# Kernel optimization log

Hardware: AMD Instinct MI355X
Metric: run time of the kernel (lower is better)

Reference implementation:

```python
import jax, jax.numpy as jnp
import numpy as np

K = 7          # kernel_size
DIL = 1        # dilation
TOPK = 8       # top_k
EPS = 1e-8     # torch cosine_similarity eps
W_SRC_POS = W_SRC_NEG = W_SIM_POS = W_SIM_NEG = 1.0


def unfold(x):
    # x: [B, C, H, W] -> [B, C, K*K, H, W]  (torch nn.Unfold ordering: c, kh, kw)
    B, C, H, W = x.shape
    pad = (K // 2) * DIL
    xp = jnp.pad(x, ((0, 0), (0, 0), (pad, pad), (pad, pad)))
    pats = [xp[:, :, i * DIL:i * DIL + H, j * DIL:j * DIL + W]
            for i in range(K) for j in range(K)]
    return jnp.stack(pats, axis=2)


def cosine_sim_feat(x):
    # local cosine similarity between each pixel and its KxK neighborhood
    unf = unfold(x)                                    # [B,C,K2,H,W]
    dot = jnp.einsum('bckhw,bchw->bkhw', unf, x)       # [B,K2,H,W]
    n_u = jnp.sqrt(jnp.sum(unf * unf, axis=1))         # [B,K2,H,W]
    n_x = jnp.sqrt(jnp.sum(x * x, axis=1))             # [B,H,W]
    return dot / (jnp.maximum(n_u, EPS) * jnp.maximum(n_x[:, None], EPS))


def masked_mean(x, mask):
    m = jnp.broadcast_to(mask, x.shape).astype(x.dtype)
    return jnp.sum(x * m) / jnp.maximum(jnp.sum(m), 1.0)


def reference(logits_trg, gt_src, x_ema, x_src, mix_masks, img_trg):
    # ---- masks ----
    ign_src = gt_src != 255                              # [B,1,H,W] bool
    ign_trg = (1.0 - mix_masks) > 0.5                    # [B,1,H,W] bool

    # ---- source pos/neg local cosine similarity ----
    sim_src = cosine_sim_feat(x_src)                     # [B,K2,H,W]
    unf_gt = unfold(gt_src.astype(jnp.float32))[:, 0].astype(jnp.int32)  # [B,K2,H,W]
    pos_pair = unf_gt == gt_src[:, 0][:, None]           # [B,K2,H,W]
    neg_pair = ~pos_pair
    src_pos = masked_mean(sim_src, pos_pair & ign_src)
    src_neg = masked_mean(sim_src, neg_pair & ign_src)

    # ---- target: cross class-agreement prob with neighbors ----
    sim_ema = cosine_sim_feat(x_ema)                     # [B,K2,H,W]
    p = jax.nn.softmax(logits_trg, axis=1)               # [B,C,H,W]
    unf_p = jax.nn.softmax(unfold(logits_trg), axis=1)   # [B,C,K2,H,W]
    cross_pos = jnp.einsum('bchw,bckhw->bkhw', p, unf_p) # [B,K2,H,W]

    # ---- top-k select over the K2 neighborhood axis ----
    s = jnp.moveaxis(sim_ema, 1, -1)                     # [B,H,W,K2]
    cp = jnp.moveaxis(cross_pos, 1, -1)                  # [B,H,W,K2]
    max_v, max_i = jax.lax.top_k(s, TOPK + 1)            # most-similar neighbors
    nmin_v, min_i = jax.lax.top_k(-s, TOPK)              # least-similar neighbors
    min_v = -nmin_v
    cpos_g = jnp.take_along_axis(cp, max_i, axis=-1)
    cneg_g = jnp.take_along_axis(1.0 - cp, min_i, axis=-1)
    loc_pos = max_v * -cpos_g
    loc_neg = (1.0 - min_v) * -cneg_g

    m_trg = jnp.moveaxis(ign_trg, 1, -1)                 # [B,H,W,1]
    loss_sim_pos = masked_mean(loc_pos, m_trg)
    loss_sim_neg = masked_mean(loc_neg, m_trg)

    return jnp.stack([-src_pos * W_SRC_POS,
                      src_neg * W_SRC_NEG,
                      loss_sim_pos * W_SIM_POS,
                      loss_sim_neg * W_SIM_NEG])


def setup_inputs() -> dict:
    key = jax.random.key(0)
    k1, k2, k3, k4, k5, k6 = jax.random.split(key, 6)
    B, C, H, W = 2, 19, 128, 128
    CH = 64
    return {
        'logits_trg': jax.random.normal(k1, (B, C, H, W), dtype=jnp.float32),
        'gt_src': jax.random.randint(k2, (B, 1, H, W), 0, C, dtype=jnp.int32),
        'x_ema': jax.random.normal(k3, (B, CH, H, W), dtype=jnp.float32),
        'x_src': jax.random.normal(k4, (B, CH, H, W), dtype=jnp.float32),
        'mix_masks': jax.random.randint(k5, (B, 1, H, W), 0, 2).astype(jnp.float32),
        'img_trg': jax.random.normal(k6, (B, 3, H, W), dtype=jnp.float32),
    }
```

## Files before the change

kernel.cpp:

```cpp
#include <hip/hip_runtime.h>
#include <math.h>

typedef unsigned short u16;
typedef unsigned int   u32;
typedef unsigned long long u64;

#define Cc   19
#define HWs  16384
#define NPIX 32768
#define FSTR 64
#define PSTR 24
#define NV   196
#define NTILE 512
#define UNIF19 0x2ABD2ABDu

typedef _Float16 h2    __attribute__((ext_vector_type(2)));
typedef _Float16 half8 __attribute__((ext_vector_type(8)));
typedef float  floatx4 __attribute__((ext_vector_type(4)));

__device__ inline float fd(u32 a, u32 b, float c) {
  h2 ha = __builtin_bit_cast(h2, a);
  h2 hb = __builtin_bit_cast(h2, b);
#if __has_builtin(__builtin_amdgcn_fdot2)
  return __builtin_amdgcn_fdot2(ha, hb, c, false);
#else
  return c + (float)ha[0] * (float)hb[0] + (float)ha[1] * (float)hb[1];
#endif
}

__device__ inline u32 pk(float a, float b) {
  h2 h; h[0] = (_Float16)a; h[1] = (_Float16)b;
  return __builtin_bit_cast(u32, h);
}

__global__ __launch_bounds__(256) void pre_kernel(
    const float* __restrict__ logits,
    const float* __restrict__ xsrc, const float* __restrict__ xema,
    u16* __restrict__ osrc, u16* __restrict__ oema, u16* __restrict__ pt) {
  __shared__ float smem[5376];
  int bid = blockIdx.x;
  int t = threadIdx.x;

  if (bid < 1024) {
    float* tile = smem;
    float* part = smem + 4160;
    float* invn = smem + 4416;
    int xb = bid & 255, b = (bid >> 8) & 1, z = bid >> 9;
    const float* in = z ? xema : xsrc;
    u16* out = z ? oema : osrc;
    int pix0 = xb * 64;
    int w = t >> 6, l = t & 63;

    const float* src = in + (size_t)b * 64 * HWs + pix0;
#pragma unroll
    for (int cc = 0; cc < 16; cc++) {
      int c = cc * 4 + w;
      tile[c * 65 + l] = src[(size_t)c * HWs + l];
    }
    __syncthreads();
    float s = 0.f;
#pragma unroll
    for (int c = w * 16; c < w * 16 + 16; c++) { float a = tile[c * 65 + l]; s += a * a; }
    part[w * 64 + l] = s;
    __syncthreads();
    if (t < 64) {
      float n = part[t] + part[64 + t] + part[128 + t] + part[192 + t];
      invn[t] = rsqrtf(fmaxf(n, 1e-16f));
    }
    __syncthreads();
    for (int i = t; i < 512; i += 256) {
      int px = i >> 3, q = i & 7;
      float iv = invn[px];
      float v[8];
#pragma unroll
      for (int k = 0; k < 8; k++) v[k] = tile[(q * 8 + k) * 65 + px] * iv;
      uint4 u = make_uint4(pk(v[0], v[1]), pk(v[2], v[3]), pk(v[4], v[5]), pk(v[6], v[7]));
      *((uint4*)(out + (size_t)(b * HWs + pix0 + px) * FSTR) + q) = u;
    }
  } else {
    float* lp = smem;
    int pb = bid - 1024;
    int gpix = pb * 256 + t;
    int b = gpix >> 14, hw = gpix & (HWs - 1);
    const float* lg = logits + (size_t)b * Cc * HWs + hw;
    float s = 0.f;
    float v[Cc];
#pragma unroll
    for (int c = 0; c < Cc; c++) { v[c] = __expf(lg[(size_t)c * HWs]); s += v[c]; }
    float inv = 1.0f / s;
#pragma unroll
    for (int c = 0; c < Cc; c++) lp[t * 21 + c] = v[c] * inv;
    __syncthreads();
    u16* ob = pt + (size_t)pb * 256 * PSTR;
    for (int i = t; i < 768; i += 256) {
      int px = i / 3, q = i - px * 3;
      float v8[8];
#pragma unroll
      for (int k = 0; k < 8; k++) {
        int c = q * 8 + k;
        v8[k] = (c < Cc) ? lp[px * 21 + c] : 0.f;
      }
      uint4 u = make_uint4(pk(v8[0], v8[1]), pk(v8[2], v8[3]), pk(v8[4], v8[5]), pk(v8[6], v8[7]));
      *((uint4*)(ob + (size_t)px * PSTR) + q) = u;
    }
  }
}

__global__ __launch_bounds__(512, 6) void st_kernel(
    const u16* __restrict__ fsrc, const u16* __restrict__ fema,
    const u16* __restrict__ pt, const int* __restrict__ gt,
    const float* __restrict__ mix, float* __restrict__ partials) {
  __shared__ uint4 fsb[1568];
  __shared__ uint4 prb[588];
  __shared__ _Float16 Csc[4][16][113];
  __shared__ int   gtt[NV];
  __shared__ float mixs[64];
  __shared__ u32   ksh[8][64];
  __shared__ float sacc[8][8];

  int bid = blockIdx.x;
  int swz = ((bid & 7) << 6) | (bid >> 3);
  int t = threadIdx.x, wv = t >> 6, lane = t & 63;
  int b  = swz >> 8;
  int th = (swz >> 4) & 15, tw = swz & 15;
  int h0 = th << 3, w0 = tw << 3;

  int nr = lane / 7, nc = lane - nr * 7;
  bool lact = lane < 49;

  const uint4* FS = (const uint4*)fsrc;
  const uint4* FE = (const uint4*)fema;

  uint4 E[4];
#pragma unroll
  for (int k = 0; k < 4; k++) {
    int i = t + k * 512;
    uint4 d = make_uint4(0u, 0u, 0u, 0u);
    if (i < 1568) {
      int vec = i >> 3, q = i & 7;
      int r = vec / 14, c = vec - r * 14;
      int gh = h0 + r - 3, gw = w0 + c - 3;
      if (((unsigned)gh < 128u) && ((unsigned)gw < 128u))
        d = FE[((size_t)((b << 14) | (gh << 7) | gw) << 3) + q];
    }
    E[k] = d;
  }

  for (int i = t; i < 1568; i += 512) {
    int vec = i >> 3, q = i & 7;
    int r = vec / 14, c = vec - r * 14;
    int gh = h0 + r - 3, gw = w0 + c - 3;
    uint4 d = make_uint4(0u, 0u, 0u, 0u);
    if (((unsigned)gh < 128u) && ((unsigned)gw < 128u))
      d = FS[((size_t)((b << 14) | (gh << 7) | gw) << 3) + q];
    fsb[(vec << 3) | (q ^ (vec & 7))] = d;
  }
  const uint4* PT3 = (const uint4*)pt;
  for (int i = t; i < 588; i += 512) {
    int vec = i / 3, q = i - vec * 3;
    int r = vec / 14, c = vec - r * 14;
    int gh = h0 + r - 3, gw = w0 + c - 3;
    uint4 d = make_uint4(UNIF19, UNIF19, UNIF19, UNIF19);
    if (((unsigned)gh < 128u) && ((unsigned)gw < 128u))
      d = PT3[(size_t)((b << 14) | (gh << 7) | gw) * 3 + q];
    prb[vec * 3 + q] = d;
  }
  for (int i = t; i < NV; i += 512) {
    int r = i / 14, c = i - r * 14;
    int gh = h0 + r - 3, gw = w0 + c - 3;
    int g = 0;
    if (((unsigned)gh < 128u) && ((unsigned)gw < 128u))
      g = gt[(b << 14) | (gh << 7) | gw];
    gtt[i] = g;
  }
  if (t < 64) {
    int r = t >> 3, c = t & 7;
    mixs[t] = mix[(b << 14) | ((h0 + r) << 7) | (w0 + c)];
  }
  __syncthreads();

  int rt = wv >> 1, hf = wv & 1;
  int p16 = lane & 15, gq = lane >> 4;
  int va = (2 * rt + (p16 >> 3) + 3) * 14 + ((p16 & 7) + 3);
  int ntiles = hf ? 3 : 4;
  int cb0 = hf ? 64 : 0;
  int vb0 = 28 * rt + cb0;

  {
    half8 a0 = __builtin_bit_cast(half8, fsb[(va << 3) | ((gq    ) ^ (va & 7))]);
    half8 a1 = __builtin_bit_cast(half8, fsb[(va << 3) | ((gq + 4) ^ (va & 7))]);
    for (int ct = 0; ct < ntiles; ct++) {
      int vb = vb0 + ct * 16 + p16;
      half8 b0 = __builtin_bit_cast(half8, fsb[(vb << 3) | ((gq    ) ^ (vb & 7))]);
      half8 b1 = __builtin_bit_cast(half8, fsb[(vb << 3) | ((gq + 4) ^ (vb & 7))]);
      floatx4 a4 = {0.f, 0.f, 0.f, 0.f};
      a4 = __builtin_amdgcn_mfma_f32_16x16x32_f16(a0, b0, a4, 0, 0, 0);
      a4 = __builtin_amdgcn_mfma_f32_16x16x32_f16(a1, b1, a4, 0, 0, 0);
      int row = gq << 2, col = cb0 + ct * 16 + p16;
#pragma unroll
      for (int r = 0; r < 4; r++) Csc[rt][row + r][col] = (_Float16)a4[r];
    }
  }
  __syncthreads();

#pragma unroll
  for (int k = 0; k < 4; k++) {
    int i = t + k * 512;
    if (i < 1568) {
      int vec = i >> 3, q = i & 7;
      fsb[(vec << 3) | (q ^ (vec & 7))] = E[k];
    }
  }

  float psum = 0, ssum = 0, posa = 0, nega = 0, pcntW = 0, vcntW = 0, cntW = 0;
  int ri = wv & 1;

  for (int tc = 0; tc < 8; ++tc) {
    int vcH = (wv + 3) * 14 + (tc + 3);
    int gtcv = gtt[vcH];
    if (gtcv != 255) {
      int cbi = lact ? ((ri + nr) * 14 + (tc + nc)) : 0;
      float sims = (float)Csc[rt][ri * 8 + tc][cbi];
      int vnH = lact ? ((wv + nr) * 14 + (tc + nc)) : vcH;
      int gtn = gtt[vnH];
      bool pos = (gtn == gtcv);
      if (lact) { ssum += sims; if (pos) psum += sims; }
      u64 mk = __ballot(lact && pos);
      pcntW += (float)__popcll(mk);
      vcntW += 1.f;
    }
  }
  __syncthreads();

  {
    half8 a0 = __builtin_bit_cast(half8, fsb[(va << 3) | ((gq    ) ^ (va & 7))]);
    half8 a1 = __builtin_bit_cast(half8, fsb[(va << 3) | ((gq + 4) ^ (va & 7))]);
    for (int ct = 0; ct < ntiles; ct++) {
      int vb = vb0 + ct * 16 + p16;
      half8 b0 = __builtin_bit_cast(half8, fsb[(vb << 3) | ((gq    ) ^ (vb & 7))]);
      half8 b1 = __builtin_bit_cast(half8, fsb[(vb << 3) | ((gq + 4) ^ (vb & 7))]);
      floatx4 a4 = {0.f, 0.f, 0.f, 0.f};
      a4 = __builtin_amdgcn_mfma_f32_16x16x32_f16(a0, b0, a4, 0, 0, 0);
      a4 = __builtin_amdgcn_mfma_f32_16x16x32_f16(a1, b1, a4, 0, 0, 0);
      int row = gq << 2, col = cb0 + ct * 16 + p16;
#pragma unroll
      for (int r = 0; r < 4; r++) Csc[rt][row + r][col] = (_Float16)a4[r];
    }
  }
  __syncthreads();

  for (int tc = 0; tc < 8; ++tc) {
    if (mixs[(wv << 3) | tc] < 0.5f) {
      int vcH = (wv + 3) * 14 + (tc + 3);
      int vnH = lact ? ((wv + nr) * 14 + (tc + nc)) : vcH;
      int cbi = lact ? ((ri + nr) * 14 + (tc + nc)) : 0;
      float v = lact ? (float)Csc[rt][ri * 8 + tc][cbi] : 0.f;

      uint4 pA = prb[vnH * 3 + 0], pB = prb[vnH * 3 + 1], pC = prb[vnH * 3 + 2];
      uint4 qA = prb[vcH * 3 + 0], qB = prb[vcH * 3 + 1], qC = prb[vcH * 3 + 2];
      float p0 = 0, p1 = 0, p2 = 0;
      p0 = fd(qA.x,pA.x,p0); p0 = fd(qA.y,pA.y,p0); p0 = fd(qA.z,pA.z,p0); p0 = fd(qA.w,pA.w,p0);
      p1 = fd(qB.x,pB.x,p1); p1 = fd(qB.y,pB.y,p1); p1 = fd(qB.z,pB.z,p1); p1 = fd(qB.w,pB.w,p1);
      p2 = fd(qC.x,pC.x,p2); p2 = fd(qC.y,pC.y,p2); p2 = fd(qC.z,pC.z,p2); p2 = fd(qC.w,pC.w,p2);
      float cp = (p0 + p1) + p2;

      u32 bits = __float_as_uint(v);
      u32 mono = (bits & 0x80000000u) ? ~bits : (bits | 0x80000000u);
      u32 key = (mono & 0xFFFFFFC0u) | (u32)lane;
      ksh[wv][lane] = key;
      int rd = 0;
      const uint4* kr = (const uint4*)ksh[wv];
#pragma unroll
      for (int j = 0; j < 12; j++) {
        uint4 qq = kr[j];
        rd += (qq.x > key); rd += (qq.y > key); rd += (qq.z > key); rd += (qq.w > key);
      }
      rd += (ksh[wv][48] > key);
      if (lact) {
        if (rd < 9)   posa += v * cp;
        if (rd >= 41) nega += (1.f - v) * (1.f - cp);
      }
      cntW += 1.f;
    }
  }

#pragma unroll
  for (int off = 32; off; off >>= 1) {
    psum += __shfl_xor(psum, off); ssum += __shfl_xor(ssum, off);
    posa += __shfl_xor(posa, off); nega += __shfl_xor(nega, off);
  }
  if (lane == 0) {
    sacc[wv][0] = psum;  sacc[wv][1] = pcntW; sacc[wv][2] = ssum;
    sacc[wv][3] = posa;  sacc[wv][4] = nega;  sacc[wv][5] = vcntW;
    sacc[wv][6] = cntW;  sacc[wv][7] = 0.f;
  }
  __syncthreads();
  if (t < 8) {
    float s = 0.f;
#pragma unroll
    for (int k = 0; k < 8; k++) s += sacc[k][t];
    partials[(size_t)bid * 8 + t] = s;
  }
}

__global__ __launch_bounds__(256) void finish_kernel(
    const float* __restrict__ partials, float* __restrict__ out) {
  int t = threadIdx.x, lane = t & 63, wv = t >> 6;
  float s0=0,s1=0,s2=0,s3=0,s4=0,s5=0,s6=0;
  for (int r = t; r < NTILE; r += 256) {
    const float4* p = (const float4*)(partials + (size_t)r * 8);
    float4 x = p[0], y = p[1];
    s0 += x.x; s1 += x.y; s2 += x.z; s3 += x.w;
    s4 += y.x; s5 += y.y; s6 += y.z;
  }
#pragma unroll
  for (int off = 32; off; off >>= 1) {
    s0 += __shfl_xor(s0, off); s1 += __shfl_xor(s1, off);
    s2 += __shfl_xor(s2, off); s3 += __shfl_xor(s3, off);
    s4 += __shfl_xor(s4, off); s5 += __shfl_xor(s5, off);
    s6 += __shfl_xor(s6, off);
  }
  __shared__ float sacc[4][8];
  if (lane == 0) {
    sacc[wv][0]=s0; sacc[wv][1]=s1; sacc[wv][2]=s2; sacc[wv][3]=s3;
    sacc[wv][4]=s4; sacc[wv][5]=s5; sacc[wv][6]=s6;
  }
  __syncthreads();
  if (t == 0) {
    float a[7];
#pragma unroll
    for (int c = 0; c < 7; c++) a[c] = sacc[0][c] + sacc[1][c] + sacc[2][c] + sacc[3][c];
    float psum = a[0], pcnt = a[1], ssum = a[2];
    float posa = a[3], nega = a[4], vcnt = a[5], cnt = a[6];
    float nsum = ssum - psum;
    float ncnt = 49.f * vcnt - pcnt;
    out[0] = -(psum / fmaxf(pcnt, 1.0f));
    out[1] =  (nsum / fmaxf(ncnt, 1.0f));
    out[2] = -(posa / fmaxf(9.0f * cnt, 1.0f));
    out[3] = -(nega / fmaxf(8.0f * cnt, 1.0f));
  }
}

extern "C" void kernel_launch(void* const* d_in, const int* in_sizes, int n_in,
                              void* d_out, int out_size, void* d_ws, size_t ws_size,
                              hipStream_t stream) {
  const float* logits = (const float*)d_in[0];
  const int*   gt     = (const int*)  d_in[1];
  const float* xema   = (const float*)d_in[2];
  const float* xsrc   = (const float*)d_in[3];
  const float* mix    = (const float*)d_in[4];
  float* out = (float*)d_out;

  float* partials = (float*)d_ws;
  u16* fsrc = (u16*)((char*)d_ws + NTILE * 8 * sizeof(float));
  u16* fema = fsrc + (size_t)NPIX * FSTR;
  u16* pt   = fema + (size_t)NPIX * FSTR;

  pre_kernel<<<1152, 256, 0, stream>>>(logits, xsrc, xema, fsrc, fema, pt);
  st_kernel<<<NTILE, 512, 0, stream>>>(fsrc, fema, pt, gt, mix, partials);
  finish_kernel<<<1, 256, 0, stream>>>(partials, out);
}
```

Before: 30.28 us.

## Compute class-agreement dot products with MFMA and pad probability stride

```diff
diff --git a/kernel.cpp b/kernel.cpp
--- a/kernel.cpp
+++ b/kernel.cpp
@@ -9,7 +9,7 @@
 #define HWs  16384
 #define NPIX 32768
 #define FSTR 64
-#define PSTR 24
+#define PSTR 32
 #define NV   196
 #define NTILE 512
 #define UNIF19 0x2ABD2ABDu
@@ -17,16 +17,6 @@
 typedef _Float16 h2    __attribute__((ext_vector_type(2)));
 typedef _Float16 half8 __attribute__((ext_vector_type(8)));
 typedef float  floatx4 __attribute__((ext_vector_type(4)));
-
-__device__ inline float fd(u32 a, u32 b, float c) {
-  h2 ha = __builtin_bit_cast(h2, a);
-  h2 hb = __builtin_bit_cast(h2, b);
-#if __has_builtin(__builtin_amdgcn_fdot2)
-  return __builtin_amdgcn_fdot2(ha, hb, c, false);
-#else
-  return c + (float)ha[0] * (float)hb[0] + (float)ha[1] * (float)hb[1];
-#endif
-}
 
 __device__ inline u32 pk(float a, float b) {
   h2 h; h[0] = (_Float16)a; h[1] = (_Float16)b;
@@ -52,10 +42,13 @@
     int w = t >> 6, l = t & 63;
 
     const float* src = in + (size_t)b * 64 * HWs + pix0;
-#pragma unroll
-    for (int cc = 0; cc < 16; cc++) {
-      int c = cc * 4 + w;
-      tile[c * 65 + l] = src[(size_t)c * HWs + l];
+    int c16 = t >> 4, px4 = (t & 15) * 4;
+#pragma unroll
+    for (int it = 0; it < 4; it++) {
+      int c = it * 16 + c16;
+      float4 v = *(const float4*)(src + (size_t)c * HWs + px4);
+      float* dst = tile + c * 65 + px4;
+      dst[0] = v.x; dst[1] = v.y; dst[2] = v.z; dst[3] = v.w;
     }
     __syncthreads();
     float s = 0.f;
@@ -92,8 +85,8 @@
     for (int c = 0; c < Cc; c++) lp[t * 21 + c] = v[c] * inv;
     __syncthreads();
     u16* ob = pt + (size_t)pb * 256 * PSTR;
-    for (int i = t; i < 768; i += 256) {
-      int px = i / 3, q = i - px * 3;
+    for (int i = t; i < 1024; i += 256) {
+      int px = i >> 2, q = i & 3;
       float v8[8];
 #pragma unroll
       for (int k = 0; k < 8; k++) {
@@ -106,13 +99,14 @@
   }
 }
 
-__global__ __launch_bounds__(512, 6) void st_kernel(
+__global__ __launch_bounds__(512, 4) void st_kernel(
     const u16* __restrict__ fsrc, const u16* __restrict__ fema,
     const u16* __restrict__ pt, const int* __restrict__ gt,
     const float* __restrict__ mix, float* __restrict__ partials) {
   __shared__ uint4 fsb[1568];
-  __shared__ uint4 prb[588];
-  __shared__ _Float16 Csc[4][16][113];
+  __shared__ uint4 prbs[784];
+  __shared__ _Float16 Cv[4][16][113];
+  __shared__ _Float16 Cp[4][16][113];
   __shared__ int   gtt[NV];
   __shared__ float mixs[64];
   __shared__ u32   ksh[8][64];
@@ -155,15 +149,15 @@
       d = FS[((size_t)((b << 14) | (gh << 7) | gw) << 3) + q];
     fsb[(vec << 3) | (q ^ (vec & 7))] = d;
   }
-  const uint4* PT3 = (const uint4*)pt;
-  for (int i = t; i < 588; i += 512) {
-    int vec = i / 3, q = i - vec * 3;
+  const uint4* PT4 = (const uint4*)pt;
+  for (int i = t; i < 784; i += 512) {
+    int vec = i >> 2, q = i & 3;
     int r = vec / 14, c = vec - r * 14;
     int gh = h0 + r - 3, gw = w0 + c - 3;
     uint4 d = make_uint4(UNIF19, UNIF19, UNIF19, UNIF19);
     if (((unsigned)gh < 128u) && ((unsigned)gw < 128u))
-      d = PT3[(size_t)((b << 14) | (gh << 7) | gw) * 3 + q];
-    prb[vec * 3 + q] = d;
+      d = PT4[((size_t)((b << 14) | (gh << 7) | gw) << 2) + q];
+    prbs[(vec << 2) | (q ^ (vec & 3))] = d;
   }
   for (int i = t; i < NV; i += 512) {
     int r = i / 14, c = i - r * 14;
@@ -198,7 +192,7 @@
       a4 = __builtin_amdgcn_mfma_f32_16x16x32_f16(a1, b1, a4, 0, 0, 0);
       int row = gq << 2, col = cb0 + ct * 16 + p16;
 #pragma unroll
-      for (int r = 0; r < 4; r++) Csc[rt][row + r][col] = (_Float16)a4[r];
+      for (int r = 0; r < 4; r++) Cv[rt][row + r][col] = (_Float16)a4[r];
     }
   }
   __syncthreads();
@@ -220,7 +214,7 @@
     int gtcv = gtt[vcH];
     if (gtcv != 255) {
       int cbi = lact ? ((ri + nr) * 14 + (tc + nc)) : 0;
-      float sims = (float)Csc[rt][ri * 8 + tc][cbi];
+      float sims = (float)Cv[rt][ri * 8 + tc][cbi];
       int vnH = lact ? ((wv + nr) * 14 + (tc + nc)) : vcH;
       int gtn = gtt[vnH];
       bool pos = (gtn == gtcv);
@@ -235,34 +229,32 @@
   {
     half8 a0 = __builtin_bit_cast(half8, fsb[(va << 3) | ((gq    ) ^ (va & 7))]);
     half8 a1 = __builtin_bit_cast(half8, fsb[(va << 3) | ((gq + 4) ^ (va & 7))]);
+    half8 ap = __builtin_bit_cast(half8, prbs[(va << 2) | (gq ^ (va & 3))]);
     for (int ct = 0; ct < ntiles; ct++) {
       int vb = vb0 + ct * 16 + p16;
       half8 b0 = __builtin_bit_cast(half8, fsb[(vb << 3) | ((gq    ) ^ (vb & 7))]);
       half8 b1 = __builtin_bit_cast(half8, fsb[(vb << 3) | ((gq + 4) ^ (vb & 7))]);
+      half8 bp = __builtin_bit_cast(half8, prbs[(vb << 2) | (gq ^ (vb & 3))]);
       floatx4 a4 = {0.f, 0.f, 0.f, 0.f};
       a4 = __builtin_amdgcn_mfma_f32_16x16x32_f16(a0, b0, a4, 0, 0, 0);
       a4 = __builtin_amdgcn_mfma_f32_16x16x32_f16(a1, b1, a4, 0, 0, 0);
+      floatx4 p4 = {0.f, 0.f, 0.f, 0.f};
+      p4 = __builtin_amdgcn_mfma_f32_16x16x32_f16(ap, bp, p4, 0, 0, 0);
       int row = gq << 2, col = cb0 + ct * 16 + p16;
 #pragma unroll
-      for (int r = 0; r < 4; r++) Csc[rt][row + r][col] = (_Float16)a4[r];
+      for (int r = 0; r < 4; r++) {
+        Cv[rt][row + r][col] = (_Float16)a4[r];
+        Cp[rt][row + r][col] = (_Float16)p4[r];
+      }
     }
   }
   __syncthreads();
 
   for (int tc = 0; tc < 8; ++tc) {
     if (mixs[(wv << 3) | tc] < 0.5f) {
-      int vcH = (wv + 3) * 14 + (tc + 3);
-      int vnH = lact ? ((wv + nr) * 14 + (tc + nc)) : vcH;
       int cbi = lact ? ((ri + nr) * 14 + (tc + nc)) : 0;
-      float v = lact ? (float)Csc[rt][ri * 8 + tc][cbi] : 0.f;
-
-      uint4 pA = prb[vnH * 3 + 0], pB = prb[vnH * 3 + 1], pC = prb[vnH * 3 + 2];
-      uint4 qA = prb[vcH * 3 + 0], qB = prb[vcH * 3 + 1], qC = prb[vcH * 3 + 2];
-      float p0 = 0, p1 = 0, p2 = 0;
-      p0 = fd(qA.x,pA.x,p0); p0 = fd(qA.y,pA.y,p0); p0 = fd(qA.z,pA.z,p0); p0 = fd(qA.w,pA.w,p0);
-      p1 = fd(qB.x,pB.x,p1); p1 = fd(qB.y,pB.y,p1); p1 = fd(qB.z,pB.z,p1); p1 = fd(qB.w,pB.w,p1);
-      p2 = fd(qC.x,pC.x,p2); p2 = fd(qC.y,pC.y,p2); p2 = fd(qC.z,pC.z,p2); p2 = fd(qC.w,pC.w,p2);
-      float cp = (p0 + p1) + p2;
+      float v  = lact ? (float)Cv[rt][ri * 8 + tc][cbi] : 0.f;
+      float cp = lact ? (float)Cp[rt][ri * 8 + tc][cbi] : 0.f;
 
       u32 bits = __float_as_uint(v);
       u32 mono = (bits & 0x80000000u) ? ~bits : (bits | 0x80000000u);
```

Measured after the change: 30.93 us. +2.1%, slower.
